# Kernel optimization log

Measured on AMD Instinct MI355X. Metric: run time of the kernel, lower is better.

## Reference

```python
import jax, jax.numpy as jnp
import numpy as np
from jax import lax

B, N = 4, 2000
PRE_NMS_LIMIT = 1000
NMS_THRESHOLD = 0.3
MAX_OUTPUT_NUM = 128
MASK_IN = 28
MASK_OUT = 32  # fixed resize target (original's per-box variable-size PIL resize is not jit-able)


def setup_inputs() -> dict:
    key = jax.random.key(0)
    k1, k2, k3, k4, k5 = jax.random.split(key, 5)
    # realistic 3D boxes inside a 128^3 volume: (y1, x1, z1, y2, x2, z2)
    ctr = jax.random.uniform(k1, (B, N, 3), minval=16.0, maxval=112.0)
    size = jax.random.uniform(k2, (B, N, 3), minval=4.0, maxval=32.0)
    proposals = jnp.concatenate([ctr - 0.5 * size, ctr + 0.5 * size], axis=-1)
    predict_scores = jax.random.uniform(k3, (B, N), dtype=jnp.float32)
    predict_deltas = 0.1 * jax.random.normal(k4, (B, N, 6), dtype=jnp.float32)
    predict_masks = jax.random.uniform(k5, (B, N, 1, MASK_IN, MASK_IN, MASK_IN), dtype=jnp.float32)
    return {"proposals": proposals, "predict_scores": predict_scores,
            "predict_deltas": predict_deltas, "predict_masks": predict_masks}


def _apply_regress_3d(deltas, boxes):
    # boxes: [K,(y1,x1,z1,y2,x2,z2)], deltas: [K,(dy,dx,dz,dh,dw,dd)]
    h = boxes[:, 3] - boxes[:, 0]
    w = boxes[:, 4] - boxes[:, 1]
    d = boxes[:, 5] - boxes[:, 2]
    cy = boxes[:, 0] + 0.5 * h + deltas[:, 0] * h
    cx = boxes[:, 1] + 0.5 * w + deltas[:, 1] * w
    cz = boxes[:, 2] + 0.5 * d + deltas[:, 2] * d
    h = h * jnp.exp(deltas[:, 3])
    w = w * jnp.exp(deltas[:, 4])
    d = d * jnp.exp(deltas[:, 5])
    return jnp.stack([cy - 0.5 * h, cx - 0.5 * w, cz - 0.5 * d,
                      cy + 0.5 * h, cx + 0.5 * w, cz + 0.5 * d], axis=-1)


def _iou_one_vs_all(box, boxes):
    # 3D IoU of one box [6] against boxes [K,6]
    iy = jnp.clip(jnp.minimum(box[3], boxes[:, 3]) - jnp.maximum(box[0], boxes[:, 0]), 0.0)
    ix = jnp.clip(jnp.minimum(box[4], boxes[:, 4]) - jnp.maximum(box[1], boxes[:, 1]), 0.0)
    iz = jnp.clip(jnp.minimum(box[5], boxes[:, 5]) - jnp.maximum(box[2], boxes[:, 2]), 0.0)
    inter = iy * ix * iz
    v1 = (box[3] - box[0]) * (box[4] - box[1]) * (box[5] - box[2])
    v2 = (boxes[:, 3] - boxes[:, 0]) * (boxes[:, 4] - boxes[:, 1]) * (boxes[:, 5] - boxes[:, 2])
    return inter / (v1 + v2 - inter + 1e-8)


def _nms_3d(bboxes, scores, thr, max_out):
    # greedy NMS: repeatedly pick highest-score unsuppressed box, suppress overlaps
    K = scores.shape[0]

    def step(suppressed, _):
        masked = jnp.where(suppressed, -jnp.inf, scores)
        idx = jnp.argmax(masked)
        valid = jnp.logical_not(suppressed[idx])
        ious = _iou_one_vs_all(bboxes[idx], bboxes)
        new_sup = suppressed | (ious > thr)
        new_sup = new_sup.at[idx].set(True)
        return new_sup, (idx, valid)

    _, (idxs, valids) = lax.scan(step, jnp.zeros((K,), dtype=bool), None, length=max_out)
    return idxs, valids  # [max_out], [max_out]


def _resize_mask(m):
    # m: [1, 28, 28, 28] -> [1, 32, 32, 32] trilinear
    return jax.image.resize(m, (1, MASK_OUT, MASK_OUT, MASK_OUT), method="trilinear")


def _detect_one(proposals_b, scores_b, deltas_b, masks_b):
    order = jnp.argsort(-scores_b)[:PRE_NMS_LIMIT]
    scores_s = scores_b[order]
    bboxes = _apply_regress_3d(deltas_b[order], proposals_b[order])
    idxs, valid = _nms_3d(bboxes, scores_s, NMS_THRESHOLD, MAX_OUTPUT_NUM)
    vf = valid.astype(bboxes.dtype)
    kept_boxes = bboxes[idxs] * vf[:, None]                       # [M,6]
    kept_masks = masks_b[order[idxs]]                             # [M,1,28,28,28]
    resized = jax.vmap(_resize_mask)(kept_masks) * vf[:, None, None, None, None]
    return kept_boxes, resized


def reference(proposals, predict_scores, predict_deltas, predict_masks):
    boxes, masks = jax.vmap(_detect_one)(proposals, predict_scores, predict_deltas, predict_masks)
    batch_bboxes = boxes.reshape(B * MAX_OUTPUT_NUM, 6)
    batch_masks = masks.reshape(B * MAX_OUTPUT_NUM, 1, MASK_OUT, MASK_OUT, MASK_OUT)
    batch_indices = jnp.repeat(jnp.arange(B, dtype=jnp.float32), MAX_OUTPUT_NUM)
    return batch_bboxes, batch_masks, batch_indices
```

## Files before the change

kernel.cpp:

```cpp
#include <hip/hip_runtime.h>
#include <stdint.h>

#define BB 4
#define NN 2000
#define K_PRE 1000
#define KPAD 1024
#define MAXOUT 128
#define NMS_THR 0.3f
#define MASK_IN_VOX (28*28*28)
#define MASK_OUT_VOX (32*32*32)

typedef float f4 __attribute__((ext_vector_type(4)));

__global__ __launch_bounds__(256) void rank_kernel(const float* __restrict__ scores,
                                                   const float* __restrict__ proposals,
                                                   const float* __restrict__ deltas,
                                                   int* __restrict__ order,
                                                   float* __restrict__ boxes_ws) {
    int b = blockIdx.x >> 5;
    int blk = blockIdx.x & 31;
    __shared__ float s[NN];
    const float* sb = scores + b * NN;
    for (int u = threadIdx.x; u < NN / 4; u += 256)
        ((float4*)s)[u] = ((const float4*)sb)[u];
    __syncthreads();

    int i = blk * 64 + (threadIdx.x >> 2);
    int q = threadIdx.x & 3;
    float si = (i < NN) ? s[i] : 0.f;
    int cnt = 0;
    int j0 = q * 500;
    const float4* s4 = (const float4*)s;
#pragma unroll 5
    for (int u = 0; u < 125; ++u) {
        float4 v = s4[j0 / 4 + u];
        int j = j0 + u * 4;
        cnt += (v.x > si) + (v.y > si) + (v.z > si) + (v.w > si);
        cnt += ((v.x == si) & (j + 0 < i)) + ((v.y == si) & (j + 1 < i))
             + ((v.z == si) & (j + 2 < i)) + ((v.w == si) & (j + 3 < i));
    }
    cnt += __shfl_xor(cnt, 1);
    cnt += __shfl_xor(cnt, 2);

    if (q == 0 && i < NN && cnt < K_PRE) {
        int rank = cnt;
        order[b * KPAD + rank] = i;
        const float* p = proposals + (size_t)(b * NN + i) * 6;
        const float* d = deltas    + (size_t)(b * NN + i) * 6;
        float py1 = p[0], px1 = p[1], pz1 = p[2], py2 = p[3], px2 = p[4], pz2 = p[5];
        float h = py2 - py1, w = px2 - px1, dd = pz2 - pz1;
        float cy = py1 + 0.5f * h + d[0] * h;
        float cx = px1 + 0.5f * w + d[1] * w;
        float cz = pz1 + 0.5f * dd + d[2] * dd;
        h *= expf(d[3]); w *= expf(d[4]); dd *= expf(d[5]);
        float* bw = boxes_ws + (size_t)b * 6 * KPAD + rank;
        bw[0 * KPAD] = cy - 0.5f * h;  bw[1 * KPAD] = cx - 0.5f * w;  bw[2 * KPAD] = cz - 0.5f * dd;
        bw[3 * KPAD] = cy + 0.5f * h;  bw[4 * KPAD] = cx + 0.5f * w;  bw[5 * KPAD] = cz + 0.5f * dd;
    }
}

__global__ __launch_bounds__(256) void build_kernel(const float* __restrict__ boxes_ws,
                                                    uint32_t* __restrict__ pairBits) {
    int b = blockIdx.y;
    int pbase = blockIdx.x * 8;
    __shared__ float sbx[6][1088];
    int tid = threadIdx.x;
    const float* bw = boxes_ws + (size_t)b * 6 * KPAD;
    for (int k = tid; k < KPAD; k += 256) {
        int ks = k + (k >> 4);
#pragma unroll
        for (int c = 0; c < 6; ++c) sbx[c][ks] = bw[c * KPAD + k];
    }
    __syncthreads();
    int l = tid & 63, lr = tid >> 6;
#pragma unroll
    for (int pss = 0; pss < 2; ++pss) {
        int p = pbase + pss * 4 + lr;
        uint32_t out = 0;
#pragma unroll
        for (int half = 0; half < 2; ++half) {
            int k = 2 * p + half;
            int ks = k + (k >> 4);
            float ry1 = sbx[0][ks], rx1 = sbx[1][ks], rz1 = sbx[2][ks];
            float ry2 = sbx[3][ks], rx2 = sbx[4][ks], rz2 = sbx[5][ks];
            float v1 = (ry2 - ry1) * (rx2 - rx1) * (rz2 - rz1);
            uint32_t bits = 0;
#pragma unroll
            for (int w = 0; w < 16; ++w) {
                int j = 64 * w + l;
                int js = j + (j >> 4);
                float y1 = sbx[0][js], x1 = sbx[1][js], z1 = sbx[2][js];
                float y2 = sbx[3][js], x2 = sbx[4][js], z2 = sbx[5][js];
                float iy = fmaxf(fminf(ry2, y2) - fmaxf(ry1, y1), 0.f);
                float ix = fmaxf(fminf(rx2, x2) - fmaxf(rx1, x1), 0.f);
                float iz = fmaxf(fminf(rz2, z2) - fmaxf(rz1, z1), 0.f);
                float inter = iy * ix * iz;
                float v2 = (y2 - y1) * (x2 - x1) * (z2 - z1);
                float iou = inter / (v1 + v2 - inter + 1e-8f);
                bits |= (iou > NMS_THR ? 1u : 0u) << w;
            }
            out |= bits << (16 * half);
        }
        if (p < K_PRE / 2)
            pairBits[((size_t)(b * 512 + p)) * 64 + l] = out;
    }
}

__global__ __launch_bounds__(512) void resize_walk_kernel(
        const float* __restrict__ masks,
        const uint32_t* __restrict__ pairBits,
        const int* __restrict__ order,
        const float* __restrict__ boxes_ws,
        float* __restrict__ out_boxes,
        float* __restrict__ out_masks,
        float* __restrict__ out_bidx) {
    int s = blockIdx.x;
    int b = s >> 7;
    int sl = s & 127;
    int tid = threadIdx.x;

    __shared__ int   res_k;
    __shared__ float res_vf;

    if (tid < 64) {
        int lane = tid;
        const uint32_t* pairB = pairBits + (size_t)b * 512 * 64;
        uint32_t sup = (lane >= 40) ? (1u << 15) : 0u;
        int nsel = 0, kmine = 0, got = 0;

        auto PAIR = [&](int p) -> uint32_t {
            return pairB[((size_t)p << 6) + lane];
        };

        for (int w = 0; w < 16 && nsel <= sl; ++w) {
            unsigned long long m = ~__ballot((int)((sup >> w) & 1u));
            while (m != 0ull && nsel <= sl) {
                unsigned long long t = m;
                int p1 = __builtin_ctzll(t) >> 1; t &= ~(3ull << (p1 * 2));
                bool h2 = t != 0; int p2 = h2 ? (__builtin_ctzll(t) >> 1) : p1; t &= ~(3ull << (p2 * 2));
                bool h3 = t != 0; int p3 = h3 ? (__builtin_ctzll(t) >> 1) : p1; t &= ~(3ull << (p3 * 2));
                bool h4 = t != 0; int p4 = h4 ? (__builtin_ctzll(t) >> 1) : p1;
                uint32_t q1 = PAIR((w << 5) + p1), q2 = PAIR((w << 5) + p2);
                uint32_t q3 = PAIR((w << 5) + p3), q4 = PAIR((w << 5) + p4);

                auto ACC = [&](uint32_t rowbits, int kbit) {
                    if (nsel <= sl && ((m >> kbit) & 1ull)) {
                        if (nsel == sl) { kmine = (w << 6) + kbit; got = 1; }
                        sup |= rowbits;
                        nsel++;
                        m = ~__ballot((int)((sup >> w) & 1u));
                    }
                };
                ACC(q1 & 0xFFFFu, 2 * p1); ACC(q1 >> 16, 2 * p1 + 1);
                if (h2) { ACC(q2 & 0xFFFFu, 2 * p2); ACC(q2 >> 16, 2 * p2 + 1); }
                if (h3) { ACC(q3 & 0xFFFFu, 2 * p3); ACC(q3 >> 16, 2 * p3 + 1); }
                if (h4) { ACC(q4 & 0xFFFFu, 2 * p4); ACC(q4 >> 16, 2 * p4 + 1); }
            }
        }
        if (lane == 0) { res_k = kmine; res_vf = got ? 1.f : 0.f; }
    }
    __syncthreads();

    int k = res_k;
    float vf = res_vf;
    int gi = order[b * KPAD + k];

    if (tid == 0) {
        const float* bw = boxes_ws + (size_t)b * 6 * KPAD;
        float* ob = out_boxes + (size_t)s * 6;
#pragma unroll
        for (int c = 0; c < 6; ++c) ob[c] = bw[c * KPAD + k] * vf;
        out_bidx[s] = (float)b;
    }

    const float* src = masks + (size_t)(b * NN + gi) * MASK_IN_VOX;
    float* dst = out_masks + (size_t)s * MASK_OUT_VOX;

    int tg = tid >> 8;
    int t8 = tid & 255;
    int q  = t8 & 7;
    int oy = t8 >> 3;

    int yf = (oy == 0) ? -1 : (14 * oy - 1) >> 4;
    float fy = (0.875f * (float)oy - 0.0625f) - (float)yf;
    int y0 = yf < 0 ? 0 : yf;
    int y1 = yf + 1 > 27 ? 27 : yf + 1;

    int ox0 = q * 4;
    int xf0 = (ox0 == 0) ? -1 : (14 * ox0 - 1) >> 4;
    int x0q = xf0 < 0 ? 0 : xf0;
    int cA = x0q >> 2;
    int cB = cA + 1 > 6 ? 6 : cA + 1;

    float W[4][8];
#pragma unroll
    for (int qq = 0; qq < 4; ++qq) {
        int ox = ox0 + qq;
        int xf = (ox == 0) ? -1 : (14 * ox - 1) >> 4;
        float fx = (0.875f * (float)ox - 0.0625f) - (float)xf;
        int x0 = xf < 0 ? 0 : xf;
        int x1 = xf + 1 > 27 ? 27 : xf + 1;
        int i0 = x0 - (cA << 2), i1 = x1 - (cA << 2);
#pragma unroll
        for (int m = 0; m < 8; ++m)
            W[qq][m] = (m == i0 ? 1.f - fx : 0.f) + (m == i1 ? fx : 0.f);
    }

    f4 W0a, W0b, W1a, W1b;
    int z0c = -9, z1c = -9;

    auto YL = [&](int z, f4& wa, f4& wb) {
        const f4* r0 = (const f4*)(src + (z * 28 + y0) * 28);
        const f4* r1 = (const f4*)(src + (z * 28 + y1) * 28);
        f4 a0 = r0[cA], a1 = r0[cB];
        f4 b0 = r1[cA], b1 = r1[cB];
        wa = a0 + fy * (b0 - a0);
        wb = a1 + fy * (b1 - a1);
    };

    int oz0 = tg * 16;
    for (int oz = oz0; oz < oz0 + 16; ++oz) {
        int zf = (oz == 0) ? -1 : (14 * oz - 1) >> 4;
        float fz = (0.875f * (float)oz - 0.0625f) - (float)zf;
        int z0 = zf < 0 ? 0 : zf;
        int z1 = zf + 1 > 27 ? 27 : zf + 1;

        if (z0 != z0c) {
            if (z0 == z1c) { W0a = W1a; W0b = W1b; }
            else           { YL(z0, W0a, W0b); }
            z0c = z0;
        }
        if (z1 != z1c) { YL(z1, W1a, W1b); z1c = z1; }

        f4 Ca = W0a + fz * (W1a - W0a);
        f4 Cb = W0b + fz * (W1b - W0b);
        float e0 = Ca.x, e1 = Ca.y, e2 = Ca.z, e3 = Ca.w;
        float e4 = Cb.x, e5 = Cb.y, e6 = Cb.z, e7 = Cb.w;

        f4 o;
#pragma unroll
        for (int qq = 0; qq < 4; ++qq) {
            float acc = W[qq][0] * e0 + W[qq][1] * e1 + W[qq][2] * e2 + W[qq][3] * e3
                      + W[qq][4] * e4 + W[qq][5] * e5 + W[qq][6] * e6 + W[qq][7] * e7;
            o[qq] = acc * vf;
        }
        __builtin_nontemporal_store(o, (f4*)(dst + oz * 1024 + oy * 32 + ox0));
    }
}

extern "C" void kernel_launch(void* const* d_in, const int* in_sizes, int n_in,
                              void* d_out, int out_size, void* d_ws, size_t ws_size,
                              hipStream_t stream) {
    const float* proposals = (const float*)d_in[0];
    const float* scores    = (const float*)d_in[1];
    const float* deltas    = (const float*)d_in[2];
    const float* masks     = (const float*)d_in[3];

    float* out = (float*)d_out;
    float* out_boxes = out;
    float* out_masks = out + (size_t)BB * MAXOUT * 6;
    float* out_bidx  = out + (size_t)BB * MAXOUT * 6 + (size_t)BB * MAXOUT * MASK_OUT_VOX;

    char* ws = (char*)d_ws;
    int*       order    = (int*)(ws);
    float*     boxes_ws = (float*)(ws + (20 << 10));
    uint32_t*  pairBits = (uint32_t*)(ws + (116 << 10));

    rank_kernel<<<BB * 32, 256, 0, stream>>>(scores, proposals, deltas, order, boxes_ws);
    build_kernel<<<dim3(64, BB), 256, 0, stream>>>(boxes_ws, pairBits);
    resize_walk_kernel<<<BB * MAXOUT, 512, 0, stream>>>(masks, pairBits, order, boxes_ws,
                                                        out_boxes, out_masks, out_bidx);
}
```

Measured before the change: 52.43 us.

## Pack four IoU rows per 64-bit word and precompute suppression ballots in NMS walk

The build kernel now packs the suppression bits of four candidate rows into one 64-bit word per lane, instead of two rows into a 32-bit word. The greedy walk therefore fetches up to 16 candidates per round of global loads. The walk also computes the four row ballots up front and updates the candidate mask with an AND-NOT, instead of re-running a ballot on the accumulated suppression state after every accepted box. This shortens the serial dependency chain and the load latency in the single-wavefront NMS walk. The cost is wider loads and extra ballots for rows that end up unused.

```diff
diff --git a/kernel.cpp b/kernel.cpp
--- a/kernel.cpp
+++ b/kernel.cpp
@@ -60,9 +60,9 @@
 }
 
 __global__ __launch_bounds__(256) void build_kernel(const float* __restrict__ boxes_ws,
-                                                    uint32_t* __restrict__ pairBits) {
+                                                    unsigned long long* __restrict__ quadBits) {
     int b = blockIdx.y;
-    int pbase = blockIdx.x * 8;
+    int pbase = blockIdx.x * 4;
     __shared__ float sbx[6][1088];
     int tid = threadIdx.x;
     const float* bw = boxes_ws + (size_t)b * 6 * KPAD;
@@ -73,42 +73,39 @@
     }
     __syncthreads();
     int l = tid & 63, lr = tid >> 6;
-#pragma unroll
-    for (int pss = 0; pss < 2; ++pss) {
-        int p = pbase + pss * 4 + lr;
-        uint32_t out = 0;
-#pragma unroll
-        for (int half = 0; half < 2; ++half) {
-            int k = 2 * p + half;
-            int ks = k + (k >> 4);
-            float ry1 = sbx[0][ks], rx1 = sbx[1][ks], rz1 = sbx[2][ks];
-            float ry2 = sbx[3][ks], rx2 = sbx[4][ks], rz2 = sbx[5][ks];
-            float v1 = (ry2 - ry1) * (rx2 - rx1) * (rz2 - rz1);
-            uint32_t bits = 0;
-#pragma unroll
-            for (int w = 0; w < 16; ++w) {
-                int j = 64 * w + l;
-                int js = j + (j >> 4);
-                float y1 = sbx[0][js], x1 = sbx[1][js], z1 = sbx[2][js];
-                float y2 = sbx[3][js], x2 = sbx[4][js], z2 = sbx[5][js];
-                float iy = fmaxf(fminf(ry2, y2) - fmaxf(ry1, y1), 0.f);
-                float ix = fmaxf(fminf(rx2, x2) - fmaxf(rx1, x1), 0.f);
-                float iz = fmaxf(fminf(rz2, z2) - fmaxf(rz1, z1), 0.f);
-                float inter = iy * ix * iz;
-                float v2 = (y2 - y1) * (x2 - x1) * (z2 - z1);
-                float iou = inter / (v1 + v2 - inter + 1e-8f);
-                bits |= (iou > NMS_THR ? 1u : 0u) << w;
-            }
-            out |= bits << (16 * half);
-        }
-        if (p < K_PRE / 2)
-            pairBits[((size_t)(b * 512 + p)) * 64 + l] = out;
-    }
+    int p = pbase + lr;
+    unsigned long long out = 0;
+#pragma unroll
+    for (int half = 0; half < 4; ++half) {
+        int k = 4 * p + half;
+        int ks = k + (k >> 4);
+        float ry1 = sbx[0][ks], rx1 = sbx[1][ks], rz1 = sbx[2][ks];
+        float ry2 = sbx[3][ks], rx2 = sbx[4][ks], rz2 = sbx[5][ks];
+        float v1 = (ry2 - ry1) * (rx2 - rx1) * (rz2 - rz1);
+        unsigned long long bits = 0;
+#pragma unroll
+        for (int w = 0; w < 16; ++w) {
+            int j = 64 * w + l;
+            int js = j + (j >> 4);
+            float y1 = sbx[0][js], x1 = sbx[1][js], z1 = sbx[2][js];
+            float y2 = sbx[3][js], x2 = sbx[4][js], z2 = sbx[5][js];
+            float iy = fmaxf(fminf(ry2, y2) - fmaxf(ry1, y1), 0.f);
+            float ix = fmaxf(fminf(rx2, x2) - fmaxf(rx1, x1), 0.f);
+            float iz = fmaxf(fminf(rz2, z2) - fmaxf(rz1, z1), 0.f);
+            float inter = iy * ix * iz;
+            float v2 = (y2 - y1) * (x2 - x1) * (z2 - z1);
+            float iou = inter / (v1 + v2 - inter + 1e-8f);
+            bits |= (unsigned long long)(iou > NMS_THR ? 1u : 0u) << w;
+        }
+        out |= bits << (16 * half);
+    }
+    if (p < K_PRE / 4)
+        quadBits[((size_t)(b * 256 + p)) * 64 + l] = out;
 }
 
 __global__ __launch_bounds__(512) void resize_walk_kernel(
         const float* __restrict__ masks,
-        const uint32_t* __restrict__ pairBits,
+        const unsigned long long* __restrict__ quadBits,
         const int* __restrict__ order,
         const float* __restrict__ boxes_ws,
         float* __restrict__ out_boxes,
@@ -124,37 +121,57 @@
 
     if (tid < 64) {
         int lane = tid;
-        const uint32_t* pairB = pairBits + (size_t)b * 512 * 64;
+        const unsigned long long* quadB = quadBits + (size_t)b * 256 * 64;
         uint32_t sup = (lane >= 40) ? (1u << 15) : 0u;
         int nsel = 0, kmine = 0, got = 0;
-
-        auto PAIR = [&](int p) -> uint32_t {
-            return pairB[((size_t)p << 6) + lane];
-        };
 
         for (int w = 0; w < 16 && nsel <= sl; ++w) {
             unsigned long long m = ~__ballot((int)((sup >> w) & 1u));
             while (m != 0ull && nsel <= sl) {
                 unsigned long long t = m;
-                int p1 = __builtin_ctzll(t) >> 1; t &= ~(3ull << (p1 * 2));
-                bool h2 = t != 0; int p2 = h2 ? (__builtin_ctzll(t) >> 1) : p1; t &= ~(3ull << (p2 * 2));
-                bool h3 = t != 0; int p3 = h3 ? (__builtin_ctzll(t) >> 1) : p1; t &= ~(3ull << (p3 * 2));
-                bool h4 = t != 0; int p4 = h4 ? (__builtin_ctzll(t) >> 1) : p1;
-                uint32_t q1 = PAIR((w << 5) + p1), q2 = PAIR((w << 5) + p2);
-                uint32_t q3 = PAIR((w << 5) + p3), q4 = PAIR((w << 5) + p4);
-
-                auto ACC = [&](uint32_t rowbits, int kbit) {
-                    if (nsel <= sl && ((m >> kbit) & 1ull)) {
-                        if (nsel == sl) { kmine = (w << 6) + kbit; got = 1; }
-                        sup |= rowbits;
-                        nsel++;
-                        m = ~__ballot((int)((sup >> w) & 1u));
-                    }
-                };
-                ACC(q1 & 0xFFFFu, 2 * p1); ACC(q1 >> 16, 2 * p1 + 1);
-                if (h2) { ACC(q2 & 0xFFFFu, 2 * p2); ACC(q2 >> 16, 2 * p2 + 1); }
-                if (h3) { ACC(q3 & 0xFFFFu, 2 * p3); ACC(q3 >> 16, 2 * p3 + 1); }
-                if (h4) { ACC(q4 & 0xFFFFu, 2 * p4); ACC(q4 >> 16, 2 * p4 + 1); }
+                int p1 = __builtin_ctzll(t) >> 2; t &= ~(0xFull << (p1 * 4));
+                bool h2 = t != 0; int p2 = h2 ? (__builtin_ctzll(t) >> 2) : p1; t &= ~(0xFull << (p2 * 4));
+                bool h3 = t != 0; int p3 = h3 ? (__builtin_ctzll(t) >> 2) : p1; t &= ~(0xFull << (p3 * 4));
+                bool h4 = t != 0; int p4 = h4 ? (__builtin_ctzll(t) >> 2) : p1;
+                unsigned long long Q1 = quadB[(((size_t)(w << 4) + p1) << 6) + lane];
+                unsigned long long Q2 = quadB[(((size_t)(w << 4) + p2) << 6) + lane];
+                unsigned long long Q3 = quadB[(((size_t)(w << 4) + p3) << 6) + lane];
+                unsigned long long Q4 = quadB[(((size_t)(w << 4) + p4) << 6) + lane];
+
+#define DOQUAD(P, Q)                                                            \
+                {                                                               \
+                    uint32_t r0 = (uint32_t)(Q) & 0xFFFFu;                      \
+                    uint32_t r1 = (uint32_t)((Q) >> 16) & 0xFFFFu;              \
+                    uint32_t r2 = (uint32_t)((Q) >> 32) & 0xFFFFu;              \
+                    uint32_t r3 = (uint32_t)((Q) >> 48) & 0xFFFFu;              \
+                    unsigned long long b0 = __ballot((int)((r0 >> w) & 1u));    \
+                    unsigned long long b1 = __ballot((int)((r1 >> w) & 1u));    \
+                    unsigned long long b2 = __ballot((int)((r2 >> w) & 1u));    \
+                    unsigned long long b3 = __ballot((int)((r3 >> w) & 1u));    \
+                    int kb = (P) * 4;                                           \
+                    if (nsel <= sl && ((m >> kb) & 1ull)) {                     \
+                        if (nsel == sl) { kmine = (w << 6) + kb; got = 1; }     \
+                        sup |= r0; nsel++; m &= ~b0;                            \
+                    }                                                           \
+                    if (nsel <= sl && ((m >> (kb + 1)) & 1ull)) {               \
+                        if (nsel == sl) { kmine = (w << 6) + kb + 1; got = 1; } \
+                        sup |= r1; nsel++; m &= ~b1;                            \
+                    }                                                           \
+                    if (nsel <= sl && ((m >> (kb + 2)) & 1ull)) {               \
+                        if (nsel == sl) { kmine = (w << 6) + kb + 2; got = 1; } \
+                        sup |= r2; nsel++; m &= ~b2;                            \
+                    }                                                           \
+                    if (nsel <= sl && ((m >> (kb + 3)) & 1ull)) {               \
+                        if (nsel == sl) { kmine = (w << 6) + kb + 3; got = 1; } \
+                        sup |= r3; nsel++; m &= ~b3;                            \
+                    }                                                           \
+                }
+
+                DOQUAD(p1, Q1)
+                if (h2) DOQUAD(p2, Q2)
+                if (h3) DOQUAD(p3, Q3)
+                if (h4) DOQUAD(p4, Q4)
+#undef DOQUAD
             }
         }
         if (lane == 0) { res_k = kmine; res_vf = got ? 1.f : 0.f; }
@@ -262,12 +279,12 @@
     float* out_bidx  = out + (size_t)BB * MAXOUT * 6 + (size_t)BB * MAXOUT * MASK_OUT_VOX;
 
     char* ws = (char*)d_ws;
-    int*       order    = (int*)(ws);
-    float*     boxes_ws = (float*)(ws + (20 << 10));
-    uint32_t*  pairBits = (uint32_t*)(ws + (116 << 10));
+    int*                 order    = (int*)(ws);
+    float*               boxes_ws = (float*)(ws + (20 << 10));
+    unsigned long long*  quadBits = (unsigned long long*)(ws + (116 << 10));
 
     rank_kernel<<<BB * 32, 256, 0, stream>>>(scores, proposals, deltas, order, boxes_ws);
-    build_kernel<<<dim3(64, BB), 256, 0, stream>>>(boxes_ws, pairBits);
-    resize_walk_kernel<<<BB * MAXOUT, 512, 0, stream>>>(masks, pairBits, order, boxes_ws,
+    build_kernel<<<dim3(64, BB), 256, 0, stream>>>(boxes_ws, quadBits);
+    resize_walk_kernel<<<BB * MAXOUT, 512, 0, stream>>>(masks, quadBits, order, boxes_ws,
                                                         out_boxes, out_masks, out_bidx);
 }
```

Result: faster. 50.02 us (-4.6%).
